# Performance work log

Measured on AMD Instinct MI355X. Metric: run time of the kernel, lower is better.

Reference implementation:

```python
import jax, jax.numpy as jnp
import numpy as np

D_MODEL = 3072
NUM_EXPERTS = 8
TOP_K = 2
BATCH, SEQ = 4, 4096


def setup_inputs() -> dict:
    key = jax.random.key(0)
    kx, kw, kb = jax.random.split(key, 3)
    x = jax.random.normal(kx, (BATCH, SEQ, D_MODEL), dtype=jnp.float32)
    W = jax.random.normal(kw, (NUM_EXPERTS, D_MODEL), dtype=jnp.float32) * (1.0 / np.sqrt(D_MODEL))
    b = jax.random.normal(kb, (NUM_EXPERTS,), dtype=jnp.float32) * 0.02
    return {"x": x, "W": W, "b": b}


def reference(x, W, b):
    # Linear gate: [B, S, D] x [E, D]^T -> [B, S, E]
    logits = jnp.einsum("bsd,ed->bse", x, W) + b
    gate_scores = jax.nn.softmax(logits, axis=-1)
    # top-k over experts
    topk_values, topk_indices = jax.lax.top_k(gate_scores, TOP_K)
    # renormalize the selected scores with a second softmax
    topk_values = jax.nn.softmax(topk_values, axis=-1)
    return (topk_values, topk_indices)
```

## Files before the change

kernel.cpp:

```cpp
#include <hip/hip_runtime.h>
#include <stdint.h>


#define NTOK   16384
#define DMODEL 3072
#define NEXP   8
#define NDB    8
#define DCH    (DMODEL / NDB)
#define DS     32
#define NST    (DCH / DS)
#define TPB    256

typedef __attribute__((address_space(1))) const void gvoid;
typedef __attribute__((address_space(3))) void lvoid;

__global__ __launch_bounds__(TPB) void gate_logits_kernel(
    const float* __restrict__ x, const float* __restrict__ W,
    float* __restrict__ logits) {
  __shared__ float4 sbuf[2][2048];

  const int tid = threadIdx.x;
  const int wave = tid >> 6;
  const int lane = tid & 63;
  const int tokBase = blockIdx.x * TPB;
  const int dBase = blockIdx.y * DCH;

  auto issue_stage = [&](int s, int b) {
    const int d0 = dBase + s * DS;
#pragma unroll
    for (int k = 0; k < 8; ++k) {
      const int c = wave * 8 + k;
      const int g = c * 64 + lane;
      const int tok = g >> 3;
      const int slot = g & 7;
      const int d4 = slot ^ (tok & 7);
      const float* gp =
          x + (size_t)(tokBase + tok) * DMODEL + d0 + d4 * 4;
      __builtin_amdgcn_global_load_lds((gvoid*)gp, (lvoid*)&sbuf[b][c * 64],
                                       16, 0, 0);
    }
  };

  float acc[NEXP];
#pragma unroll
  for (int e = 0; e < NEXP; ++e) acc[e] = 0.f;

  issue_stage(0, 0);
  issue_stage(1, 1);

  for (int s = 0; s < NST; ++s) {
    if (s < NST - 1) {
      asm volatile("s_waitcnt vmcnt(8)\n\ts_barrier" ::: "memory");
    } else {
      asm volatile("s_waitcnt vmcnt(0)\n\ts_barrier" ::: "memory");
    }

    const int b = s & 1;
    const int d0 = dBase + s * DS;
    const float4* row = &sbuf[b][tid * 8];
#pragma unroll
    for (int q = 0; q < 8; ++q) {
      const float4 xv = row[q ^ (tid & 7)];
      const int dw = d0 + q * 4;
#pragma unroll
      for (int e = 0; e < NEXP; ++e) {
        const float* wr = &W[e * DMODEL + dw];
        acc[e] = fmaf(xv.x, wr[0],
                 fmaf(xv.y, wr[1],
                 fmaf(xv.z, wr[2],
                 fmaf(xv.w, wr[3], acc[e]))));
      }
    }

    asm volatile("s_waitcnt lgkmcnt(0)\n\ts_barrier" ::: "memory");
    if (s + 2 < NST) issue_stage(s + 2, b);
  }

#pragma unroll
  for (int e = 0; e < NEXP; ++e) {
    atomicAdd(&logits[(size_t)(tokBase + tid) * NEXP + e], acc[e]);
  }
}

__global__ __launch_bounds__(64) void gate_topk_kernel(
    const float* __restrict__ logits, const float* __restrict__ bias,
    float* __restrict__ out) {
  const int t = blockIdx.x * 64 + threadIdx.x;
  if (t >= NTOK) return;

  float l[NEXP];
#pragma unroll
  for (int e = 0; e < NEXP; ++e) l[e] = logits[(size_t)t * NEXP + e] + bias[e];

  float m = l[0];
#pragma unroll
  for (int e = 1; e < NEXP; ++e) m = fmaxf(m, l[e]);

  float p[NEXP];
  float ssum = 0.f;
#pragma unroll
  for (int e = 0; e < NEXP; ++e) {
    p[e] = expf(l[e] - m);
    ssum += p[e];
  }
  const float inv = 1.f / ssum;
#pragma unroll
  for (int e = 0; e < NEXP; ++e) p[e] *= inv;

  int i1 = 0;
  float v1 = p[0];
#pragma unroll
  for (int e = 1; e < NEXP; ++e) {
    if (p[e] > v1) { v1 = p[e]; i1 = e; }
  }
  int i2 = -1;
  float v2 = -1.f;
#pragma unroll
  for (int e = 0; e < NEXP; ++e) {
    if (e == i1) continue;
    if (p[e] > v2) { v2 = p[e]; i2 = e; }
  }

  const float e2 = expf(v2 - v1);
  const float r = 1.f / (1.f + e2);

  out[(size_t)t * 2 + 0] = r;
  out[(size_t)t * 2 + 1] = e2 * r;
  out[2 * NTOK + (size_t)t * 2 + 0] = (float)i1;
  out[2 * NTOK + (size_t)t * 2 + 1] = (float)i2;
}

extern "C" void kernel_launch(void* const* d_in, const int* in_sizes, int n_in,
                              void* d_out, int out_size, void* d_ws,
                              size_t ws_size, hipStream_t stream) {
  const float* x = (const float*)d_in[0];
  const float* W = (const float*)d_in[1];
  const float* b = (const float*)d_in[2];
  float* out = (float*)d_out;
  float* logits = (float*)d_ws;

  hipMemsetAsync(d_ws, 0, (size_t)NTOK * NEXP * sizeof(float), stream);

  dim3 grid1(NTOK / TPB, NDB);
  gate_logits_kernel<<<grid1, TPB, 0, stream>>>(x, W, logits);

  gate_topk_kernel<<<NTOK / 64, 64, 0, stream>>>(logits, b, out);
}
```

Measured before the change: 338.2 us.

## Stage W slice in LDS and give each wave private x buffers

```diff
diff --git a/kernel.cpp b/kernel.cpp
--- a/kernel.cpp
+++ b/kernel.cpp
@@ -17,69 +17,106 @@
 __global__ __launch_bounds__(TPB) void gate_logits_kernel(
     const float* __restrict__ x, const float* __restrict__ W,
     float* __restrict__ logits) {
-  __shared__ float4 sbuf[2][2048];
+  __shared__ float4 sx[4][2][512];
+  __shared__ float sw[NEXP * DCH];
 
   const int tid = threadIdx.x;
-  const int wave = tid >> 6;
+  const int wv = tid >> 6;
   const int lane = tid & 63;
+  const int sl = lane >> 3;
+  const int tg = lane & 7;
   const int tokBase = blockIdx.x * TPB;
   const int dBase = blockIdx.y * DCH;
 
-  auto issue_stage = [&](int s, int b) {
-    const int d0 = dBase + s * DS;
+  for (int f = tid; f < NEXP * DCH / 4; f += TPB) {
+    const int e = f / (DCH / 4);
+    const int j = f % (DCH / 4);
+    const float4 v = *(const float4*)&W[e * DMODEL + dBase + j * 4];
+    *(float4*)&sw[e * DCH + j * 4] = v;
+  }
+  __syncthreads();
+
+  const float* xw = x + (size_t)(tokBase + wv * 64) * DMODEL + dBase;
+
+  auto issue = [&](int s, int b) {
+    const int d0 = s * DS;
 #pragma unroll
     for (int k = 0; k < 8; ++k) {
-      const int c = wave * 8 + k;
-      const int g = c * 64 + lane;
+      const int g = k * 64 + lane;
       const int tok = g >> 3;
       const int slot = g & 7;
-      const int d4 = slot ^ (tok & 7);
-      const float* gp =
-          x + (size_t)(tokBase + tok) * DMODEL + d0 + d4 * 4;
-      __builtin_amdgcn_global_load_lds((gvoid*)gp, (lvoid*)&sbuf[b][c * 64],
+      const float* gp = xw + (size_t)tok * DMODEL + d0 + slot * 4;
+      __builtin_amdgcn_global_load_lds((gvoid*)gp, (lvoid*)&sx[wv][b][k * 64],
                                        16, 0, 0);
     }
   };
 
-  float acc[NEXP];
+  float acc[8][NEXP];
 #pragma unroll
-  for (int e = 0; e < NEXP; ++e) acc[e] = 0.f;
+  for (int p = 0; p < 8; ++p)
+#pragma unroll
+    for (int e = 0; e < NEXP; ++e) acc[p][e] = 0.f;
 
-  issue_stage(0, 0);
-  issue_stage(1, 1);
+  issue(0, 0);
+  issue(1, 1);
 
+#pragma unroll 2
   for (int s = 0; s < NST; ++s) {
-    if (s < NST - 1) {
-      asm volatile("s_waitcnt vmcnt(8)\n\ts_barrier" ::: "memory");
+    if (s == NST - 1) {
+      asm volatile("s_waitcnt vmcnt(0)" ::: "memory");
     } else {
-      asm volatile("s_waitcnt vmcnt(0)\n\ts_barrier" ::: "memory");
+      asm volatile("s_waitcnt vmcnt(8)" ::: "memory");
     }
 
     const int b = s & 1;
-    const int d0 = dBase + s * DS;
-    const float4* row = &sbuf[b][tid * 8];
+
+    float4 w4[NEXP];
 #pragma unroll
-    for (int q = 0; q < 8; ++q) {
-      const float4 xv = row[q ^ (tid & 7)];
-      const int dw = d0 + q * 4;
+    for (int e = 0; e < NEXP; ++e)
+      w4[e] = *(const float4*)&sw[e * DCH + s * DS + sl * 4];
+
+    const float4* buf = sx[wv][b];
+#pragma unroll
+    for (int p = 0; p < 8; ++p) {
+      const float4 xv = buf[(p * 8 + tg) * 8 + sl];
 #pragma unroll
       for (int e = 0; e < NEXP; ++e) {
-        const float* wr = &W[e * DMODEL + dw];
-        acc[e] = fmaf(xv.x, wr[0],
-                 fmaf(xv.y, wr[1],
-                 fmaf(xv.z, wr[2],
-                 fmaf(xv.w, wr[3], acc[e]))));
+        acc[p][e] = fmaf(xv.x, w4[e].x,
+                    fmaf(xv.y, w4[e].y,
+                    fmaf(xv.z, w4[e].z,
+                    fmaf(xv.w, w4[e].w, acc[p][e]))));
       }
     }
 
-    asm volatile("s_waitcnt lgkmcnt(0)\n\ts_barrier" ::: "memory");
-    if (s + 2 < NST) issue_stage(s + 2, b);
+    if (s + 2 < NST) {
+      asm volatile("s_waitcnt lgkmcnt(0)" ::: "memory");
+      issue(s + 2, b);
+    }
   }
 
 #pragma unroll
-  for (int e = 0; e < NEXP; ++e) {
-    atomicAdd(&logits[(size_t)(tokBase + tid) * NEXP + e], acc[e]);
+  for (int p = 0; p < 8; ++p)
+#pragma unroll
+    for (int e = 0; e < NEXP; ++e) {
+      float v = acc[p][e];
+      v += __shfl_xor(v, 8, 64);
+      v += __shfl_xor(v, 16, 64);
+      v += __shfl_xor(v, 32, 64);
+      acc[p][e] = v;
+    }
+
+  float out8[NEXP];
+#pragma unroll
+  for (int p = 0; p < 8; ++p) {
+    if (p == sl) {
+#pragma unroll
+      for (int e = 0; e < NEXP; ++e) out8[e] = acc[p][e];
+    }
   }
+
+  float* lp = &logits[(size_t)(tokBase + wv * 64 + lane) * NEXP];
+#pragma unroll
+  for (int e = 0; e < NEXP; ++e) atomicAdd(lp + e, out8[e]);
 }
 
 __global__ __launch_bounds__(64) void gate_topk_kernel(
```

Result: faster. 296.8 us (-12.2%).
